# Kernel tuning notes

Hardware: AMD Instinct MI355X
Metric: run time of the kernel (lower is better)

Reference implementation:

```python
import jax, jax.numpy as jnp
import numpy as np

N = 16384      # total atoms (8 proteins x ~2048)
E = 524288     # N * max_neighbors(32)
B = 8          # graphs
F_IN = 26      # 20 residue types + 6 atom types
D = 128        # node_dim
H = 256        # hidden_dim
OUT = 64       # output_dim
L = 4          # n_layers
N_RBF = 16
CUTOFF = 10.0


def setup_inputs() -> dict:
    key = jax.random.key(0)
    ks = jax.random.split(key, 24)
    s = 0.05
    inp = {
        "positions": jax.random.normal(ks[0], (N, 3), jnp.float32) * 10.0,
        "node_features": jax.random.normal(ks[1], (N, F_IN), jnp.float32),
        "edge_index": jax.random.randint(ks[2], (2, E), 0, N, jnp.int32),
        "batch": jnp.sort(jax.random.randint(ks[3], (N,), 0, B, jnp.int32)),
        # node embedding MLP
        "emb_W1": jax.random.normal(ks[4], (F_IN, D), jnp.float32) * s,
        "emb_b1": jnp.zeros((D,), jnp.float32),
        "emb_W2": jax.random.normal(ks[5], (D, D), jnp.float32) * s,
        "emb_b2": jnp.zeros((D,), jnp.float32),
        # per-layer message MLP: [2D + n_rbf] -> H -> D
        "msg_W1": jax.random.normal(ks[6], (L, 2 * D + N_RBF, H), jnp.float32) * s,
        "msg_b1": jnp.zeros((L, H), jnp.float32),
        "msg_W2": jax.random.normal(ks[7], (L, H, D), jnp.float32) * s,
        "msg_b2": jnp.zeros((L, D), jnp.float32),
        # per-layer update MLP: [2D] -> H -> D (residual)
        "upd_W1": jax.random.normal(ks[8], (L, 2 * D, H), jnp.float32) * s,
        "upd_b1": jnp.zeros((L, H), jnp.float32),
        "upd_W2": jax.random.normal(ks[9], (L, H, D), jnp.float32) * s,
        "upd_b2": jnp.zeros((L, D), jnp.float32),
        # readout MLP: D -> H -> OUT
        "r_W1": jax.random.normal(ks[10], (D, H), jnp.float32) * s,
        "r_b1": jnp.zeros((H,), jnp.float32),
        "r_W2": jax.random.normal(ks[11], (H, OUT), jnp.float32) * s,
        "r_b2": jnp.zeros((OUT,), jnp.float32),
    }
    return inp


def _mlp2(x, W1, b1, W2, b2):
    return jax.nn.silu(x @ W1 + b1) @ W2 + b2


def _edge_rbf(positions, src, dst):
    rel = positions[dst] - positions[src]                      # (E,3)
    d = jnp.sqrt(jnp.sum(rel * rel, axis=-1) + 1e-12)          # (E,)
    centers = jnp.linspace(0.0, CUTOFF, N_RBF, dtype=positions.dtype)
    width = CUTOFF / N_RBF
    rbf = jnp.exp(-((d[:, None] - centers) ** 2) / (2.0 * width * width))  # (E,n_rbf)
    env = 0.5 * (jnp.cos(jnp.pi * d / CUTOFF) + 1.0) * (d < CUTOFF)        # cosine cutoff
    return rbf * env[:, None]


def reference(positions, node_features, edge_index, batch,
              emb_W1, emb_b1, emb_W2, emb_b2,
              msg_W1, msg_b1, msg_W2, msg_b2,
              upd_W1, upd_b1, upd_W2, upd_b2,
              r_W1, r_b1, r_W2, r_b2):
    src, dst = edge_index[0], edge_index[1]
    h = _mlp2(node_features, emb_W1, emb_b1, emb_W2, emb_b2)   # (N,D)
    ef = _edge_rbf(positions, src, dst)                        # (E,n_rbf)
    for i in range(L):
        m_in = jnp.concatenate([h[src], h[dst], ef], axis=-1)  # (E,2D+n_rbf)
        m = _mlp2(m_in, msg_W1[i], msg_b1[i], msg_W2[i], msg_b2[i])  # (E,D)
        agg = jax.ops.segment_sum(m, dst, num_segments=N)      # (N,D)
        u_in = jnp.concatenate([h, agg], axis=-1)              # (N,2D)
        h = h + _mlp2(u_in, upd_W1[i], upd_b1[i], upd_W2[i], upd_b2[i])
    # mean readout per graph
    counts = jax.ops.segment_sum(jnp.ones((N,), h.dtype), batch, num_segments=B)
    g = jax.ops.segment_sum(h, batch, num_segments=B) / jnp.maximum(counts, 1.0)[:, None]
    return _mlp2(g, r_W1, r_b1, r_W2, r_b2)                    # (B,OUT)
```

## Files before the change

### kernel.cpp

```cpp
#include <hip/hip_runtime.h>
#include <math.h>

#define NATOMS 16384
#define NEDGES 524288
#define NLAYERS 4
#define TE 64

typedef __bf16 bf16x8 __attribute__((ext_vector_type(8)));
typedef __bf16 bf16x4 __attribute__((ext_vector_type(4)));
typedef float f32x4 __attribute__((ext_vector_type(4)));

__device__ __forceinline__ float silu_f(float x) {
  return x * __builtin_amdgcn_rcpf(1.0f + __expf(-x));
}

__global__ __launch_bounds__(256) void hist_kernel(
    const int* __restrict__ dst, int* __restrict__ counts)
{
  int e = blockIdx.x * 256 + threadIdx.x;
  atomicAdd(&counts[dst[e]], 1);
}

__global__ __launch_bounds__(1024) void scan_kernel(
    const int* __restrict__ counts, int* __restrict__ cursor)
{
  __shared__ int buf[1024];
  __shared__ int carry_s;
  int tid = threadIdx.x;
  if (tid == 0) carry_s = 0;
  __syncthreads();
  for (int c = 0; c < 16; c++) {
    int v = counts[c * 1024 + tid];
    buf[tid] = v;
    __syncthreads();
    for (int off = 1; off < 1024; off <<= 1) {
      int t = (tid >= off) ? buf[tid - off] : 0;
      __syncthreads();
      buf[tid] += t;
      __syncthreads();
    }
    cursor[c * 1024 + tid] = buf[tid] - v + carry_s;
    __syncthreads();
    if (tid == 1023) carry_s += buf[1023];
    __syncthreads();
  }
}

__global__ __launch_bounds__(256) void scatter_kernel(
    const int* __restrict__ src, const int* __restrict__ dst,
    int* __restrict__ cursor, int* __restrict__ esrc, int* __restrict__ edst)
{
  int e = blockIdx.x * 256 + threadIdx.x;
  int d = dst[e];
  int p = atomicAdd(&cursor[d], 1);
  esrc[p] = src[e];
  edst[p] = d;
}

__global__ __launch_bounds__(256) void degf_kernel(
    const int* __restrict__ counts, float* __restrict__ degf)
{
  int n = blockIdx.x * 256 + threadIdx.x;
  degf[n] = (float)counts[n];
}

__global__ __launch_bounds__(256) void conv_t_kernel(
    const float* __restrict__ W, __bf16* __restrict__ Wt,
    int ldN, int k0, int Kin, int Kpad, long lsrc, long ldst)
{
  long l = blockIdx.y;
  int i = blockIdx.x * 256 + threadIdx.x;
  int n = i / Kpad, k = i - n * Kpad;
  float v = (k < Kin) ? W[l * lsrc + (size_t)(k0 + k) * ldN + n] : 0.0f;
  Wt[l * ldst + (size_t)n * Kpad + k] = (__bf16)v;
}

__global__ __launch_bounds__(256) void build_b2c_kernel(
    const float* __restrict__ mW1, __bf16* __restrict__ Bc)
{
  long l = blockIdx.y;
  int i = blockIdx.x * 256 + threadIdx.x;
  int c = i >> 5, k = i & 31;
  float v = (k < 16) ? mW1[l * (272L * 256) + (size_t)(256 + k) * 256 + c] : 0.0f;
  Bc[l * (256L * 32) + i] = (__bf16)v;
}

__global__ __launch_bounds__(256) void w2u_kernel(
    const float* __restrict__ mW2, const float* __restrict__ uW1,
    float* __restrict__ W2u)
{
  long l = blockIdx.y;
  int r = blockIdx.x, c = threadIdx.x;
  float acc = 0.0f;
  for (int k = 0; k < 128; k++)
    acc += mW2[(l * 256 + r) * 128 + k] *
           uW1[l * 65536 + (size_t)(128 + k) * 256 + c];
  W2u[(l * 256 + r) * 256 + c] = acc;
}

__global__ __launch_bounds__(256) void b2u_kernel(
    const float* __restrict__ mb2, const float* __restrict__ uW1,
    float* __restrict__ b2u)
{
  long l = blockIdx.x;
  int c = threadIdx.x;
  float acc = 0.0f;
  for (int k = 0; k < 128; k++)
    acc += mb2[l * 128 + k] * uW1[l * 65536 + (size_t)(128 + k) * 256 + c];
  b2u[l * 256 + c] = acc;
}

__global__ __launch_bounds__(256) void build_uw1ft_kernel(
    const float* __restrict__ uW1, const float* __restrict__ W2u,
    __bf16* __restrict__ Wt)
{
  long l = blockIdx.y;
  int i = blockIdx.x * 256 + threadIdx.x;
  int n = i / 384, k = i - n * 384;
  float v = (k < 128) ? uW1[l * 65536 + (size_t)k * 256 + n]
                      : W2u[l * 65536 + (size_t)(k - 128) * 256 + n];
  Wt[l * (256L * 384) + i] = (__bf16)v;
}

__global__ __launch_bounds__(128) void embed_kernel(
    const float* __restrict__ x, const float* __restrict__ W1,
    const float* __restrict__ b1, const float* __restrict__ W2,
    const float* __restrict__ b2, float* __restrict__ h,
    __bf16* __restrict__ hb)
{
  int n = blockIdx.x;
  int j = threadIdx.x;
  __shared__ float xs[26];
  __shared__ float hid[128];
  if (j < 26) xs[j] = x[n * 26 + j];
  __syncthreads();
  float acc = b1[j];
  #pragma unroll
  for (int k = 0; k < 26; k++) acc += xs[k] * W1[k * 128 + j];
  hid[j] = silu_f(acc);
  __syncthreads();
  float acc2 = b2[j];
  #pragma unroll 8
  for (int k = 0; k < 128; k++) acc2 += hid[k] * W2[k * 128 + j];
  h[(size_t)n * 128 + j] = acc2;
  hb[(size_t)n * 128 + j] = (__bf16)acc2;
}

__global__ __launch_bounds__(256) void rbf_kernel(
    const float* __restrict__ pos, const int* __restrict__ esrc,
    const int* __restrict__ edst, __bf16* __restrict__ efb)
{
  int e = blockIdx.x * 256 + threadIdx.x;
  int s = esrc[e], d = edst[e];
  float dx = pos[d * 3 + 0] - pos[s * 3 + 0];
  float dy = pos[d * 3 + 1] - pos[s * 3 + 1];
  float dz = pos[d * 3 + 2] - pos[s * 3 + 2];
  float dist = sqrtf(dx * dx + dy * dy + dz * dz + 1e-12f);
  float env = (dist < 10.0f)
                  ? 0.5f * (cosf(3.14159265358979f * dist * 0.1f) + 1.0f)
                  : 0.0f;
  bf16x8 o0, o1;
  #pragma unroll
  for (int i = 0; i < 16; i++) {
    float c = (10.0f / 15.0f) * (float)i;
    float t = dist - c;
    float v = env * __expf(-t * t * 1.28f);
    if (i < 8) o0[i] = (__bf16)v; else o1[i - 8] = (__bf16)v;
  }
  *(bf16x8*)(efb + (size_t)e * 16 + 0) = o0;
  *(bf16x8*)(efb + (size_t)e * 16 + 8) = o1;
}

__global__ __launch_bounds__(256) void zprep_kernel(
    const __bf16* __restrict__ hb, const float* __restrict__ b1,
    const __bf16* __restrict__ W1at, const __bf16* __restrict__ W1bt,
    __bf16* __restrict__ z1b, __bf16* __restrict__ z2b, float* __restrict__ aggH)
{
  __shared__ __bf16 s_n[64][136];
  int tid = threadIdx.x, n0 = blockIdx.x * 64;
  {
    int n = tid >> 2, t4 = tid & 3;
    const bf16x8* hr = (const bf16x8*)(hb + (size_t)(n0 + n) * 128);
    #pragma unroll
    for (int i = 0; i < 4; i++)
      *(bf16x8*)&s_n[n][t4 * 8 + 32 * i] = hr[t4 + 4 * i];
  }
  {
    float4 zz = make_float4(0.f, 0.f, 0.f, 0.f);
    float4* ap = (float4*)(aggH + (size_t)n0 * 256);
    for (int i = tid; i < 64 * 256 / 4; i += 256) ap[i] = zz;
  }
  __syncthreads();
  const int wv = tid >> 6, ln = tid & 63, lc = ln & 15, qd = ln >> 4;
  for (int cp = 0; cp < 2; cp++) {
    f32x4 aA[4][2], aB[4][2];
    #pragma unroll
    for (int nt = 0; nt < 2; nt++) {
      float bv = b1[cp * 128 + wv * 32 + nt * 16 + lc];
      #pragma unroll
      for (int mt = 0; mt < 4; mt++) {
        aA[mt][nt][0] = 0.f; aA[mt][nt][1] = 0.f;
        aA[mt][nt][2] = 0.f; aA[mt][nt][3] = 0.f;
        aB[mt][nt][0] = bv; aB[mt][nt][1] = bv;
        aB[mt][nt][2] = bv; aB[mt][nt][3] = bv;
      }
    }
    #pragma unroll
    for (int kt = 0; kt < 4; kt++) {
      bf16x8 af[4];
      #pragma unroll
      for (int mt = 0; mt < 4; mt++)
        af[mt] = *(const bf16x8*)&s_n[mt * 16 + lc][kt * 32 + qd * 8];
      bf16x8 bwA[2], bwB[2];
      #pragma unroll
      for (int nt = 0; nt < 2; nt++) {
        int c = cp * 128 + wv * 32 + nt * 16 + lc;
        bwA[nt] = *(const bf16x8*)(W1at + (size_t)c * 128 + kt * 32 + qd * 8);
        bwB[nt] = *(const bf16x8*)(W1bt + (size_t)c * 128 + kt * 32 + qd * 8);
      }
      #pragma unroll
      for (int mt = 0; mt < 4; mt++)
        #pragma unroll
        for (int nt = 0; nt < 2; nt++) {
          aA[mt][nt] = __builtin_amdgcn_mfma_f32_16x16x32_bf16(af[mt], bwA[nt], aA[mt][nt], 0, 0, 0);
          aB[mt][nt] = __builtin_amdgcn_mfma_f32_16x16x32_bf16(af[mt], bwB[nt], aB[mt][nt], 0, 0, 0);
        }
    }
    #pragma unroll
    for (int mt = 0; mt < 4; mt++)
      #pragma unroll
      for (int nt = 0; nt < 2; nt++) {
        int c = cp * 128 + wv * 32 + nt * 16 + lc;
        #pragma unroll
        for (int r = 0; r < 4; r++) {
          int n = n0 + mt * 16 + qd * 4 + r;
          z1b[(size_t)n * 256 + c] = (__bf16)aA[mt][nt][r];
          z2b[(size_t)n * 256 + c] = (__bf16)aB[mt][nt][r];
        }
      }
  }
}

#define MS_EF_OFF   33792
#define MS_SRC_OFF  36864
#define MS_DST_OFF  37120
#define MS_MASK_OFF 37376
#define MS_BYTES    37392

__global__ __launch_bounds__(256, 4) void msg_mfma_kernel(
    const __bf16* __restrict__ z1b, const __bf16* __restrict__ z2b,
    const __bf16* __restrict__ efb,
    const int* __restrict__ esrc, const int* __restrict__ edst,
    const __bf16* __restrict__ B2c, float* __restrict__ aggH)
{
  __shared__ __align__(16) char smem[MS_BYTES];
  float (*s_hT)[66] = (float(*)[66])(smem);
  __bf16 (*s_ef)[24] = (__bf16(*)[24])(smem + MS_EF_OFF);
  int* s_src = (int*)(smem + MS_SRC_OFF);
  int* s_dst = (int*)(smem + MS_DST_OFF);
  unsigned int* s_mask = (unsigned int*)(smem + MS_MASK_OFF);

  int tid = threadIdx.x, e0 = blockIdx.x * TE;

  if (tid < TE) {
    int d = edst[e0 + tid];
    s_dst[tid] = d;
    int dp = (tid == 0) ? (d ^ 1) : edst[e0 + tid - 1];
    unsigned long long mb = __ballot(d != dp);
    if (tid == 0) { s_mask[0] = (unsigned int)mb; s_mask[1] = (unsigned int)(mb >> 32); }
  } else if (tid < 2 * TE) {
    s_src[tid - TE] = esrc[e0 + tid - TE];
  }
  {
    int e = tid >> 2, t4 = tid & 3;
    if (t4 < 2)
      *(bf16x8*)&s_ef[e][t4 * 8] =
          *(const bf16x8*)(efb + (size_t)(e0 + e) * 16 + t4 * 8);
  }
  __syncthreads();

  const int wv = tid >> 6, ln = tid & 63, lc = ln & 15, qd = ln >> 4;
  const unsigned int mlo = __builtin_amdgcn_readfirstlane(s_mask[0]);
  const unsigned int mhi = __builtin_amdgcn_readfirstlane(s_mask[1]);

  bf16x8 bI;
  #pragma unroll
  for (int j = 0; j < 8; j++)
    bI[j] = (__bf16)((lc == (qd & 1) * 8 + j) ? 1.0f : 0.0f);

  const __bf16* pz[4];
  #pragma unroll
  for (int mt = 0; mt < 4; mt++) {
    int m = mt * 16 + lc;
    int row = (qd < 2) ? s_src[m] : s_dst[m];
    pz[mt] = ((qd < 2) ? z1b : z2b) + (size_t)row * 256 + (qd & 1) * 8;
  }
  const int jcol = tid & 127, r0 = (tid >> 7) * 32;

  for (int hf = 0; hf < 2; hf++) {
    const int cb = hf * 128 + wv * 32;
    bf16x8 bw[2];
    #pragma unroll
    for (int nt = 0; nt < 2; nt++)
      bw[nt] = *(const bf16x8*)(B2c + (size_t)(cb + nt * 16 + lc) * 32 + qd * 8);

    #pragma unroll
    for (int mt = 0; mt < 4; mt++) {
      bf16x8 aef = *(const bf16x8*)&s_ef[mt * 16 + lc][(qd & 1) * 8];
      #pragma unroll
      for (int nt = 0; nt < 2; nt++) {
        bf16x8 az = *(const bf16x8*)(pz[mt] + cb + nt * 16);
        f32x4 z; z[0] = 0.f; z[1] = 0.f; z[2] = 0.f; z[3] = 0.f;
        f32x4 acc = __builtin_amdgcn_mfma_f32_16x16x32_bf16(az, bI, z, 0, 0, 0);
        acc = __builtin_amdgcn_mfma_f32_16x16x32_bf16(aef, bw[nt], acc, 0, 0, 0);
        float2 p0, p1;
        p0.x = silu_f(acc[0]); p0.y = silu_f(acc[1]);
        p1.x = silu_f(acc[2]); p1.y = silu_f(acc[3]);
        float* wp = &s_hT[wv * 32 + nt * 16 + lc][mt * 16 + qd * 4];
        *(float2*)wp = p0;
        *(float2*)(wp + 2) = p1;
      }
    }
    __syncthreads();

    {
      float2 v[16];
      #pragma unroll
      for (int c = 0; c < 16; c++)
        v[c] = *(const float2*)&s_hT[jcol][r0 + c * 2];
      float acc = 0.0f;
      int cur = s_dst[r0];
      #pragma unroll
      for (int i = 0; i < 32; i++) {
        int m = r0 + i;
        bool bnd = (m < 32) ? ((mlo >> m) & 1u) : ((mhi >> (m - 32)) & 1u);
        if (i > 0 && bnd) {
          atomicAdd(&aggH[(size_t)cur * 256 + hf * 128 + jcol], acc);
          acc = 0.0f;
          cur = s_dst[m];
        }
        acc += (i & 1) ? v[i >> 1].y : v[i >> 1].x;
      }
      atomicAdd(&aggH[(size_t)cur * 256 + hf * 128 + jcol], acc);
    }
    __syncthreads();
  }
}

__global__ __launch_bounds__(256, 2) void upd_mfma_kernel(
    float* __restrict__ h, __bf16* __restrict__ hb,
    float* __restrict__ aggH, const float* __restrict__ degf,
    const __bf16* __restrict__ uW1ft, const float* __restrict__ b1,
    const float* __restrict__ b2u,
    const __bf16* __restrict__ uW2t, const float* __restrict__ b2,
    int do_z, const float* __restrict__ nb1,
    const __bf16* __restrict__ nW1at, const __bf16* __restrict__ nW1bt,
    __bf16* __restrict__ z1b, __bf16* __restrict__ z2b)
{
  __shared__ __bf16 s_u[64][392];
  __shared__ __bf16 s_uh[64][136];
  int tid = threadIdx.x, n0 = blockIdx.x * 64;
  {
    int n = tid >> 2, t4 = tid & 3;
    const bf16x8* hr = (const bf16x8*)(hb + (size_t)(n0 + n) * 128);
    #pragma unroll
    for (int i = 0; i < 4; i++)
      *(bf16x8*)&s_u[n][t4 * 8 + 32 * i] = hr[t4 + 4 * i];
    const float* sr = aggH + (size_t)(n0 + n) * 256;
    #pragma unroll
    for (int i = 0; i < 8; i++) {
      int col = t4 * 8 + i * 32;
      float4 a = *(const float4*)(sr + col);
      float4 b = *(const float4*)(sr + col + 4);
      bf16x8 o;
      o[0] = (__bf16)a.x; o[1] = (__bf16)a.y; o[2] = (__bf16)a.z; o[3] = (__bf16)a.w;
      o[4] = (__bf16)b.x; o[5] = (__bf16)b.y; o[6] = (__bf16)b.z; o[7] = (__bf16)b.w;
      *(bf16x8*)&s_u[n][128 + col] = o;
    }
  }
  __syncthreads();
  const int wv = tid >> 6, ln = tid & 63, lc = ln & 15, qd = ln >> 4;

  float dg[4][4];
  #pragma unroll
  for (int mt = 0; mt < 4; mt++)
    #pragma unroll
    for (int r = 0; r < 4; r++)
      dg[mt][r] = degf[n0 + mt * 16 + qd * 4 + r];

  f32x4 acc2[4][2];
  #pragma unroll
  for (int nt = 0; nt < 2; nt++) {
    float bv = b2[wv * 32 + nt * 16 + lc];
    #pragma unroll
    for (int mt = 0; mt < 4; mt++) {
      acc2[mt][nt][0] = bv; acc2[mt][nt][1] = bv;
      acc2[mt][nt][2] = bv; acc2[mt][nt][3] = bv;
    }
  }

  for (int hf = 0; hf < 2; hf++) {
    f32x4 acc1[4][2];
    #pragma unroll
    for (int nt = 0; nt < 2; nt++) {
      int c = hf * 128 + wv * 32 + nt * 16 + lc;
      float bv = b1[c];
      float b2uv = b2u[c];
      #pragma unroll
      for (int mt = 0; mt < 4; mt++)
        #pragma unroll
        for (int r = 0; r < 4; r++)
          acc1[mt][nt][r] = bv + dg[mt][r] * b2uv;
    }
    #pragma unroll
    for (int kt = 0; kt < 12; kt++) {
      bf16x8 af[4];
      #pragma unroll
      for (int mt = 0; mt < 4; mt++)
        af[mt] = *(const bf16x8*)&s_u[mt * 16 + lc][kt * 32 + qd * 8];
      bf16x8 bw[2];
      #pragma unroll
      for (int nt = 0; nt < 2; nt++)
        bw[nt] = *(const bf16x8*)(uW1ft +
                 (size_t)(hf * 128 + wv * 32 + nt * 16 + lc) * 384 + kt * 32 + qd * 8);
      #pragma unroll
      for (int mt = 0; mt < 4; mt++)
        #pragma unroll
        for (int nt = 0; nt < 2; nt++)
          acc1[mt][nt] = __builtin_amdgcn_mfma_f32_16x16x32_bf16(af[mt], bw[nt], acc1[mt][nt], 0, 0, 0);
    }
    __syncthreads();
    #pragma unroll
    for (int mt = 0; mt < 4; mt++)
      #pragma unroll
      for (int nt = 0; nt < 2; nt++) {
        int cc = wv * 32 + nt * 16 + lc;
        #pragma unroll
        for (int r = 0; r < 4; r++)
          s_uh[mt * 16 + qd * 4 + r][cc] = (__bf16)silu_f(acc1[mt][nt][r]);
      }
    __syncthreads();
    #pragma unroll
    for (int kt = 0; kt < 4; kt++) {
      bf16x8 a2[4];
      #pragma unroll
      for (int mt = 0; mt < 4; mt++)
        a2[mt] = *(const bf16x8*)&s_uh[mt * 16 + lc][kt * 32 + qd * 8];
      bf16x8 b2w[2];
      #pragma unroll
      for (int nt = 0; nt < 2; nt++)
        b2w[nt] = *(const bf16x8*)(uW2t +
                  (size_t)(wv * 32 + nt * 16 + lc) * 256 + hf * 128 + kt * 32 + qd * 8);
      #pragma unroll
      for (int mt = 0; mt < 4; mt++)
        #pragma unroll
        for (int nt = 0; nt < 2; nt++)
          acc2[mt][nt] = __builtin_amdgcn_mfma_f32_16x16x32_bf16(a2[mt], b2w[nt], acc2[mt][nt], 0, 0, 0);
    }
  }

  #pragma unroll
  for (int mt = 0; mt < 4; mt++)
    #pragma unroll
    for (int nt = 0; nt < 2; nt++) {
      int c = wv * 32 + nt * 16 + lc;
      #pragma unroll
      for (int r = 0; r < 4; r++) {
        int n = n0 + mt * 16 + qd * 4 + r;
        float v = h[(size_t)n * 128 + c] + acc2[mt][nt][r];
        h[(size_t)n * 128 + c] = v;
        hb[(size_t)n * 128 + c] = (__bf16)v;
      }
    }

  if (do_z) {
    __syncthreads();
    {
      float4 zz = make_float4(0.f, 0.f, 0.f, 0.f);
      float4* ap = (float4*)(aggH + (size_t)n0 * 256);
      for (int i = tid; i < 64 * 256 / 4; i += 256) ap[i] = zz;
      int n = tid >> 2, t4 = tid & 3;
      const bf16x8* hr = (const bf16x8*)(hb + (size_t)(n0 + n) * 128);
      #pragma unroll
      for (int i = 0; i < 4; i++)
        *(bf16x8*)&s_u[n][t4 * 8 + 32 * i] = hr[t4 + 4 * i];
    }
    __syncthreads();
    for (int cp = 0; cp < 2; cp++) {
      f32x4 aA[4][2], aB[4][2];
      #pragma unroll
      for (int nt = 0; nt < 2; nt++) {
        float bv = nb1[cp * 128 + wv * 32 + nt * 16 + lc];
        #pragma unroll
        for (int mt = 0; mt < 4; mt++) {
          aA[mt][nt][0] = 0.f; aA[mt][nt][1] = 0.f;
          aA[mt][nt][2] = 0.f; aA[mt][nt][3] = 0.f;
          aB[mt][nt][0] = bv; aB[mt][nt][1] = bv;
          aB[mt][nt][2] = bv; aB[mt][nt][3] = bv;
        }
      }
      #pragma unroll
      for (int kt = 0; kt < 4; kt++) {
        bf16x8 af[4];
        #pragma unroll
        for (int mt = 0; mt < 4; mt++)
          af[mt] = *(const bf16x8*)&s_u[mt * 16 + lc][kt * 32 + qd * 8];
        bf16x8 bwA[2], bwB[2];
        #pragma unroll
        for (int nt = 0; nt < 2; nt++) {
          int c = cp * 128 + wv * 32 + nt * 16 + lc;
          bwA[nt] = *(const bf16x8*)(nW1at + (size_t)c * 128 + kt * 32 + qd * 8);
          bwB[nt] = *(const bf16x8*)(nW1bt + (size_t)c * 128 + kt * 32 + qd * 8);
        }
        #pragma unroll
        for (int mt = 0; mt < 4; mt++)
          #pragma unroll
          for (int nt = 0; nt < 2; nt++) {
            aA[mt][nt] = __builtin_amdgcn_mfma_f32_16x16x32_bf16(af[mt], bwA[nt], aA[mt][nt], 0, 0, 0);
            aB[mt][nt] = __builtin_amdgcn_mfma_f32_16x16x32_bf16(af[mt], bwB[nt], aB[mt][nt], 0, 0, 0);
          }
      }
      #pragma unroll
      for (int mt = 0; mt < 4; mt++)
        #pragma unroll
        for (int nt = 0; nt < 2; nt++) {
          int c = cp * 128 + wv * 32 + nt * 16 + lc;
          #pragma unroll
          for (int r = 0; r < 4; r++) {
            int n = n0 + mt * 16 + qd * 4 + r;
            z1b[(size_t)n * 256 + c] = (__bf16)aA[mt][nt][r];
            z2b[(size_t)n * 256 + c] = (__bf16)aB[mt][nt][r];
          }
        }
    }
  }
}

__global__ __launch_bounds__(128) void readout_sum_kernel(
    const float* __restrict__ h, const int* __restrict__ batch,
    float* __restrict__ gsum, float* __restrict__ gcnt)
{
  int j = threadIdx.x;
  int n0 = blockIdx.x * 128;
  float acc = 0.f, cacc = 0.f;
  int cur = batch[n0];
  for (int i = 0; i < 128; i++) {
    int b = batch[n0 + i];
    if (b != cur) {
      atomicAdd(&gsum[cur * 128 + j], acc);
      if (j == 0) atomicAdd(&gcnt[cur], cacc);
      acc = 0.f; cacc = 0.f; cur = b;
    }
    acc += h[(size_t)(n0 + i) * 128 + j];
    cacc += 1.f;
  }
  atomicAdd(&gsum[cur * 128 + j], acc);
  if (j == 0) atomicAdd(&gcnt[cur], cacc);
}

__global__ __launch_bounds__(256) void readout_mlp_kernel(
    const float* __restrict__ gsum, const float* __restrict__ gcnt,
    const float* __restrict__ W1, const float* __restrict__ b1,
    const float* __restrict__ W2, const float* __restrict__ b2,
    float* __restrict__ out)
{
  __shared__ float g[8][128];
  __shared__ float hid[8][256];
  int tid = threadIdx.x;
  for (int i = tid; i < 8 * 128; i += 256) {
    int b = i >> 7, c = i & 127;
    g[b][c] = gsum[i] / fmaxf(gcnt[b], 1.0f);
  }
  __syncthreads();
  {
    float bb = b1[tid];
    float a[8];
    #pragma unroll
    for (int b = 0; b < 8; b++) a[b] = bb;
    for (int k = 0; k < 128; k++) {
      float w = W1[k * 256 + tid];
      #pragma unroll
      for (int b = 0; b < 8; b++) a[b] += g[b][k] * w;
    }
    #pragma unroll
    for (int b = 0; b < 8; b++) hid[b][tid] = silu_f(a[b]);
  }
  __syncthreads();
  int j = tid & 63, bg = tid >> 6;
  float a0 = b2[j], a1 = b2[j];
  for (int k = 0; k < 256; k++) {
    float w = W2[k * 64 + j];
    a0 += hid[bg * 2 + 0][k] * w;
    a1 += hid[bg * 2 + 1][k] * w;
  }
  out[(bg * 2 + 0) * 64 + j] = a0;
  out[(bg * 2 + 1) * 64 + j] = a1;
}

extern "C" void kernel_launch(void* const* d_in, const int* in_sizes, int n_in,
                              void* d_out, int out_size, void* d_ws, size_t ws_size,
                              hipStream_t stream) {
  const float* pos   = (const float*)d_in[0];
  const float* xfeat = (const float*)d_in[1];
  const int*   eidx  = (const int*)d_in[2];
  const int*   batch = (const int*)d_in[3];
  const float* eW1 = (const float*)d_in[4];
  const float* eb1 = (const float*)d_in[5];
  const float* eW2 = (const float*)d_in[6];
  const float* eb2 = (const float*)d_in[7];
  const float* mW1 = (const float*)d_in[8];
  const float* mb1 = (const float*)d_in[9];
  const float* mW2 = (const float*)d_in[10];
  const float* mb2 = (const float*)d_in[11];
  const float* uW1 = (const float*)d_in[12];
  const float* ub1 = (const float*)d_in[13];
  const float* uW2 = (const float*)d_in[14];
  const float* ub2 = (const float*)d_in[15];
  const float* rW1 = (const float*)d_in[16];
  const float* rb1 = (const float*)d_in[17];
  const float* rW2 = (const float*)d_in[18];
  const float* rb2 = (const float*)d_in[19];

  const int* srcI = eidx;
  const int* dstI = eidx + NEDGES;

  char* base = (char*)d_ws;
  float* h    = (float*)base;  base += (size_t)NATOMS * 128 * 4;
  float* aggH = (float*)base;  base += (size_t)NATOMS * 256 * 4;
  __bf16* z1b = (__bf16*)base; base += (size_t)NATOMS * 256 * 2;
  __bf16* z2b = (__bf16*)base; base += (size_t)NATOMS * 256 * 2;
  __bf16* hb  = (__bf16*)base; base += (size_t)NATOMS * 128 * 2;
  __bf16* efb = (__bf16*)base; base += (size_t)NEDGES * 16 * 2;
  __bf16* W1at = (__bf16*)base; base += (size_t)NLAYERS * 256 * 128 * 2;
  __bf16* W1bt = (__bf16*)base; base += (size_t)NLAYERS * 256 * 128 * 2;
  __bf16* B2c  = (__bf16*)base; base += (size_t)NLAYERS * 256 * 32 * 2;
  __bf16* uW1ft = (__bf16*)base; base += (size_t)NLAYERS * 256 * 384 * 2;
  __bf16* uW2t = (__bf16*)base; base += (size_t)NLAYERS * 128 * 256 * 2;
  float* W2u  = (float*)base;  base += (size_t)NLAYERS * 256 * 256 * 4;
  float* b2u  = (float*)base;  base += (size_t)NLAYERS * 256 * 4;
  float* degf = (float*)base;  base += (size_t)NATOMS * 4;
  float* gsum = (float*)base;  base += 8 * 128 * 4;
  float* gcnt = (float*)base;  base += 8 * 4;
  int* counts = (int*)base;    base += (size_t)NATOMS * 4;
  int* cursor = (int*)base;    base += (size_t)NATOMS * 4;
  int* esrc   = (int*)base;    base += (size_t)NEDGES * 4;
  int* edst   = (int*)base;    base += (size_t)NEDGES * 4;

  hipMemsetAsync(counts, 0, NATOMS * sizeof(int), stream);
  hist_kernel<<<NEDGES / 256, 256, 0, stream>>>(dstI, counts);
  scan_kernel<<<1, 1024, 0, stream>>>(counts, cursor);
  scatter_kernel<<<NEDGES / 256, 256, 0, stream>>>(srcI, dstI, cursor, esrc, edst);
  degf_kernel<<<NATOMS / 256, 256, 0, stream>>>(counts, degf);

  conv_t_kernel<<<dim3(128, NLAYERS), 256, 0, stream>>>(mW1, W1at, 256,   0, 128, 128, 272L*256, 256L*128);
  conv_t_kernel<<<dim3(128, NLAYERS), 256, 0, stream>>>(mW1, W1bt, 256, 128, 128, 128, 272L*256, 256L*128);
  build_b2c_kernel<<<dim3(32, NLAYERS), 256, 0, stream>>>(mW1, B2c);
  w2u_kernel<<<dim3(256, NLAYERS), 256, 0, stream>>>(mW2, uW1, W2u);
  b2u_kernel<<<NLAYERS, 256, 0, stream>>>(mb2, uW1, b2u);
  build_uw1ft_kernel<<<dim3(384, NLAYERS), 256, 0, stream>>>(uW1, W2u, uW1ft);
  conv_t_kernel<<<dim3(128, NLAYERS), 256, 0, stream>>>(uW2, uW2t, 128,   0, 256, 256, 256L*128, 128L*256);

  embed_kernel<<<NATOMS, 128, 0, stream>>>(xfeat, eW1, eb1, eW2, eb2, h, hb);
  rbf_kernel<<<NEDGES / 256, 256, 0, stream>>>(pos, esrc, edst, efb);

  zprep_kernel<<<NATOMS / 64, 256, 0, stream>>>(
      hb, mb1, W1at, W1bt, z1b, z2b, aggH);

  for (int l = 0; l < NLAYERS; l++) {
    int ln = (l < NLAYERS - 1) ? (l + 1) : l;
    msg_mfma_kernel<<<NEDGES / TE, 256, 0, stream>>>(
        z1b, z2b, efb, esrc, edst,
        B2c + (size_t)l * 256 * 32, aggH);
    upd_mfma_kernel<<<NATOMS / 64, 256, 0, stream>>>(
        h, hb, aggH, degf,
        uW1ft + (size_t)l * 256 * 384, ub1 + (size_t)l * 256,
        b2u + (size_t)l * 256,
        uW2t + (size_t)l * 128 * 256, ub2 + (size_t)l * 128,
        (l < NLAYERS - 1) ? 1 : 0,
        mb1 + (size_t)ln * 256,
        W1at + (size_t)ln * 256 * 128, W1bt + (size_t)ln * 256 * 128,
        z1b, z2b);
  }

  hipMemsetAsync(gsum, 0, (8 * 128 + 8) * sizeof(float), stream);
  readout_sum_kernel<<<NATOMS / 128, 128, 0, stream>>>(h, batch, gsum, gcnt);
  readout_mlp_kernel<<<1, 256, 0, stream>>>(gsum, gcnt, rW1, rb1, rW2, rb2,
                                            (float*)d_out);
}
```

Measured before the change: 715.0 us.

## Merge weight-prep kernels, fold degree into scan, prefetch z rows, shrink upd LDS

Seven weight preparation kernels are merged into one block-partitioned prep kernel, and the W2u intermediate buffer is dropped by computing it inline. The scan now does a single-pass blocked prefix sum that also writes degf, which removes a kernel. The message kernel preloads all z gather loads into registers before the MFMA loop. The update kernel reads h directly from global memory instead of staging it in LDS, which cuts LDS use so occupancy can rise to 3 blocks. The aims are fewer launches and better latency hiding, at the cost of more registers and uncached global reads in the update GEMM.

```diff
diff --git a/kernel.cpp b/kernel.cpp
--- a/kernel.cpp
+++ b/kernel.cpp
@@ -22,27 +22,37 @@
 }
 
 __global__ __launch_bounds__(1024) void scan_kernel(
-    const int* __restrict__ counts, int* __restrict__ cursor)
-{
-  __shared__ int buf[1024];
-  __shared__ int carry_s;
+    const int* __restrict__ counts, int* __restrict__ cursor,
+    float* __restrict__ degf)
+{
+  __shared__ int s_tot[1024];
   int tid = threadIdx.x;
-  if (tid == 0) carry_s = 0;
-  __syncthreads();
-  for (int c = 0; c < 16; c++) {
-    int v = counts[c * 1024 + tid];
-    buf[tid] = v;
+  int v[16];
+  {
+    const int4* cp = (const int4*)(counts + tid * 16);
+    int4 a = cp[0], b = cp[1], c = cp[2], d = cp[3];
+    v[0]=a.x; v[1]=a.y; v[2]=a.z; v[3]=a.w;
+    v[4]=b.x; v[5]=b.y; v[6]=b.z; v[7]=b.w;
+    v[8]=c.x; v[9]=c.y; v[10]=c.z; v[11]=c.w;
+    v[12]=d.x; v[13]=d.y; v[14]=d.z; v[15]=d.w;
+  }
+  int tot = 0;
+  #pragma unroll
+  for (int i = 0; i < 16; i++) tot += v[i];
+  s_tot[tid] = tot;
+  __syncthreads();
+  for (int off = 1; off < 1024; off <<= 1) {
+    int t = (tid >= off) ? s_tot[tid - off] : 0;
     __syncthreads();
-    for (int off = 1; off < 1024; off <<= 1) {
-      int t = (tid >= off) ? buf[tid - off] : 0;
-      __syncthreads();
-      buf[tid] += t;
-      __syncthreads();
-    }
-    cursor[c * 1024 + tid] = buf[tid] - v + carry_s;
+    s_tot[tid] += t;
     __syncthreads();
-    if (tid == 1023) carry_s += buf[1023];
-    __syncthreads();
+  }
+  int run = s_tot[tid] - tot;
+  #pragma unroll
+  for (int i = 0; i < 16; i++) {
+    cursor[tid * 16 + i] = run;
+    degf[tid * 16 + i] = (float)v[i];
+    run += v[i];
   }
 }
 
@@ -57,69 +67,53 @@
   edst[p] = d;
 }
 
-__global__ __launch_bounds__(256) void degf_kernel(
-    const int* __restrict__ counts, float* __restrict__ degf)
-{
-  int n = blockIdx.x * 256 + threadIdx.x;
-  degf[n] = (float)counts[n];
-}
-
-__global__ __launch_bounds__(256) void conv_t_kernel(
-    const float* __restrict__ W, __bf16* __restrict__ Wt,
-    int ldN, int k0, int Kin, int Kpad, long lsrc, long ldst)
+__global__ __launch_bounds__(256) void prep_kernel(
+    const float* __restrict__ mW1, const float* __restrict__ mW2,
+    const float* __restrict__ uW1, const float* __restrict__ uW2,
+    const float* __restrict__ mb2,
+    __bf16* __restrict__ W1at, __bf16* __restrict__ W1bt,
+    __bf16* __restrict__ B2c, __bf16* __restrict__ uW1ft,
+    __bf16* __restrict__ uW2t, float* __restrict__ b2u)
 {
   long l = blockIdx.y;
-  int i = blockIdx.x * 256 + threadIdx.x;
-  int n = i / Kpad, k = i - n * Kpad;
-  float v = (k < Kin) ? W[l * lsrc + (size_t)(k0 + k) * ldN + n] : 0.0f;
-  Wt[l * ldst + (size_t)n * Kpad + k] = (__bf16)v;
-}
-
-__global__ __launch_bounds__(256) void build_b2c_kernel(
-    const float* __restrict__ mW1, __bf16* __restrict__ Bc)
-{
-  long l = blockIdx.y;
-  int i = blockIdx.x * 256 + threadIdx.x;
-  int c = i >> 5, k = i & 31;
-  float v = (k < 16) ? mW1[l * (272L * 256) + (size_t)(256 + k) * 256 + c] : 0.0f;
-  Bc[l * (256L * 32) + i] = (__bf16)v;
-}
-
-__global__ __launch_bounds__(256) void w2u_kernel(
-    const float* __restrict__ mW2, const float* __restrict__ uW1,
-    float* __restrict__ W2u)
-{
-  long l = blockIdx.y;
-  int r = blockIdx.x, c = threadIdx.x;
-  float acc = 0.0f;
-  for (int k = 0; k < 128; k++)
-    acc += mW2[(l * 256 + r) * 128 + k] *
-           uW1[l * 65536 + (size_t)(128 + k) * 256 + c];
-  W2u[(l * 256 + r) * 256 + c] = acc;
-}
-
-__global__ __launch_bounds__(256) void b2u_kernel(
-    const float* __restrict__ mb2, const float* __restrict__ uW1,
-    float* __restrict__ b2u)
-{
-  long l = blockIdx.x;
-  int c = threadIdx.x;
-  float acc = 0.0f;
-  for (int k = 0; k < 128; k++)
-    acc += mb2[l * 128 + k] * uW1[l * 65536 + (size_t)(128 + k) * 256 + c];
-  b2u[l * 256 + c] = acc;
-}
-
-__global__ __launch_bounds__(256) void build_uw1ft_kernel(
-    const float* __restrict__ uW1, const float* __restrict__ W2u,
-    __bf16* __restrict__ Wt)
-{
-  long l = blockIdx.y;
-  int i = blockIdx.x * 256 + threadIdx.x;
-  int n = i / 384, k = i - n * 384;
-  float v = (k < 128) ? uW1[l * 65536 + (size_t)k * 256 + n]
-                      : W2u[l * 65536 + (size_t)(k - 128) * 256 + n];
-  Wt[l * (256L * 384) + i] = (__bf16)v;
+  int bx = blockIdx.x, tid = threadIdx.x;
+  if (bx < 128) {
+    int i = bx * 256 + tid;
+    int n = i >> 7, k = i & 127;
+    W1at[l * (256L * 128) + i] = (__bf16)mW1[l * (272L * 256) + (size_t)k * 256 + n];
+  } else if (bx < 256) {
+    int i = (bx - 128) * 256 + tid;
+    int n = i >> 7, k = i & 127;
+    W1bt[l * (256L * 128) + i] = (__bf16)mW1[l * (272L * 256) + (size_t)(128 + k) * 256 + n];
+  } else if (bx < 288) {
+    int i = (bx - 256) * 256 + tid;
+    int c = i >> 5, k = i & 31;
+    float v = (k < 16) ? mW1[l * (272L * 256) + (size_t)(256 + k) * 256 + c] : 0.0f;
+    B2c[l * (256L * 32) + i] = (__bf16)v;
+  } else if (bx < 672) {
+    int i = (bx - 288) * 256 + tid;
+    int n = i / 384, k = i - n * 384;
+    float v;
+    if (k < 128) {
+      v = uW1[l * 65536 + (size_t)k * 256 + n];
+    } else {
+      int r = k - 128;
+      v = 0.0f;
+      for (int j = 0; j < 128; j++)
+        v += mW2[(l * 256 + r) * 128 + j] * uW1[l * 65536 + (size_t)(128 + j) * 256 + n];
+    }
+    uW1ft[l * (256L * 384) + i] = (__bf16)v;
+  } else if (bx < 800) {
+    int i = (bx - 672) * 256 + tid;
+    int n = i >> 8, k = i & 255;
+    uW2t[l * (128L * 256) + i] = (__bf16)uW2[l * (256L * 128) + (size_t)k * 128 + n];
+  } else {
+    int c = tid;
+    float acc = 0.0f;
+    for (int j = 0; j < 128; j++)
+      acc += mb2[l * 128 + j] * uW1[l * 65536 + (size_t)(128 + j) * 256 + c];
+    b2u[l * 256 + c] = acc;
+  }
 }
 
 __global__ __launch_bounds__(128) void embed_kernel(
@@ -288,15 +282,27 @@
   for (int j = 0; j < 8; j++)
     bI[j] = (__bf16)((lc == (qd & 1) * 8 + j) ? 1.0f : 0.0f);
 
-  const __bf16* pz[4];
-  #pragma unroll
-  for (int mt = 0; mt < 4; mt++) {
-    int m = mt * 16 + lc;
-    int row = (qd < 2) ? s_src[m] : s_dst[m];
-    pz[mt] = ((qd < 2) ? z1b : z2b) + (size_t)row * 256 + (qd & 1) * 8;
-  }
+  bf16x8 za[2][4][2];
+  {
+    const __bf16* pz[4];
+    #pragma unroll
+    for (int mt = 0; mt < 4; mt++) {
+      int m = mt * 16 + lc;
+      int row = (qd < 2) ? s_src[m] : s_dst[m];
+      pz[mt] = ((qd < 2) ? z1b : z2b) + (size_t)row * 256 + (qd & 1) * 8;
+    }
+    #pragma unroll
+    for (int hf = 0; hf < 2; hf++)
+      #pragma unroll
+      for (int mt = 0; mt < 4; mt++)
+        #pragma unroll
+        for (int nt = 0; nt < 2; nt++)
+          za[hf][mt][nt] = *(const bf16x8*)(pz[mt] + hf * 128 + wv * 32 + nt * 16);
+  }
+
   const int jcol = tid & 127, r0 = (tid >> 7) * 32;
 
+  #pragma unroll
   for (int hf = 0; hf < 2; hf++) {
     const int cb = hf * 128 + wv * 32;
     bf16x8 bw[2];
@@ -309,9 +315,8 @@
       bf16x8 aef = *(const bf16x8*)&s_ef[mt * 16 + lc][(qd & 1) * 8];
       #pragma unroll
       for (int nt = 0; nt < 2; nt++) {
-        bf16x8 az = *(const bf16x8*)(pz[mt] + cb + nt * 16);
         f32x4 z; z[0] = 0.f; z[1] = 0.f; z[2] = 0.f; z[3] = 0.f;
-        f32x4 acc = __builtin_amdgcn_mfma_f32_16x16x32_bf16(az, bI, z, 0, 0, 0);
+        f32x4 acc = __builtin_amdgcn_mfma_f32_16x16x32_bf16(za[hf][mt][nt], bI, z, 0, 0, 0);
         acc = __builtin_amdgcn_mfma_f32_16x16x32_bf16(aef, bw[nt], acc, 0, 0, 0);
         float2 p0, p1;
         p0.x = silu_f(acc[0]); p0.y = silu_f(acc[1]);
@@ -347,7 +352,7 @@
   }
 }
 
-__global__ __launch_bounds__(256, 2) void upd_mfma_kernel(
+__global__ __launch_bounds__(256, 3) void upd_mfma_kernel(
     float* __restrict__ h, __bf16* __restrict__ hb,
     float* __restrict__ aggH, const float* __restrict__ degf,
     const __bf16* __restrict__ uW1ft, const float* __restrict__ b1,
@@ -357,15 +362,11 @@
     const __bf16* __restrict__ nW1at, const __bf16* __restrict__ nW1bt,
     __bf16* __restrict__ z1b, __bf16* __restrict__ z2b)
 {
-  __shared__ __bf16 s_u[64][392];
+  __shared__ __bf16 s_s[64][264];
   __shared__ __bf16 s_uh[64][136];
   int tid = threadIdx.x, n0 = blockIdx.x * 64;
   {
     int n = tid >> 2, t4 = tid & 3;
-    const bf16x8* hr = (const bf16x8*)(hb + (size_t)(n0 + n) * 128);
-    #pragma unroll
-    for (int i = 0; i < 4; i++)
-      *(bf16x8*)&s_u[n][t4 * 8 + 32 * i] = hr[t4 + 4 * i];
     const float* sr = aggH + (size_t)(n0 + n) * 256;
     #pragma unroll
     for (int i = 0; i < 8; i++) {
@@ -375,11 +376,16 @@
       bf16x8 o;
       o[0] = (__bf16)a.x; o[1] = (__bf16)a.y; o[2] = (__bf16)a.z; o[3] = (__bf16)a.w;
       o[4] = (__bf16)b.x; o[5] = (__bf16)b.y; o[6] = (__bf16)b.z; o[7] = (__bf16)b.w;
-      *(bf16x8*)&s_u[n][128 + col] = o;
+      *(bf16x8*)&s_s[n][col] = o;
     }
   }
   __syncthreads();
   const int wv = tid >> 6, ln = tid & 63, lc = ln & 15, qd = ln >> 4;
+
+  const __bf16* ph[4];
+  #pragma unroll
+  for (int mt = 0; mt < 4; mt++)
+    ph[mt] = hb + (size_t)(n0 + mt * 16 + lc) * 128 + qd * 8;
 
   float dg[4][4];
   #pragma unroll
@@ -417,7 +423,9 @@
       bf16x8 af[4];
       #pragma unroll
       for (int mt = 0; mt < 4; mt++)
-        af[mt] = *(const bf16x8*)&s_u[mt * 16 + lc][kt * 32 + qd * 8];
+        af[mt] = (kt < 4)
+            ? *(const bf16x8*)(ph[mt] + kt * 32)
+            : *(const bf16x8*)&s_s[mt * 16 + lc][(kt - 4) * 32 + qd * 8];
       bf16x8 bw[2];
       #pragma unroll
       for (int nt = 0; nt < 2; nt++)
@@ -479,13 +487,7 @@
       float4 zz = make_float4(0.f, 0.f, 0.f, 0.f);
       float4* ap = (float4*)(aggH + (size_t)n0 * 256);
       for (int i = tid; i < 64 * 256 / 4; i += 256) ap[i] = zz;
-      int n = tid >> 2, t4 = tid & 3;
-      const bf16x8* hr = (const bf16x8*)(hb + (size_t)(n0 + n) * 128);
-      #pragma unroll
-      for (int i = 0; i < 4; i++)
-        *(bf16x8*)&s_u[n][t4 * 8 + 32 * i] = hr[t4 + 4 * i];
-    }
-    __syncthreads();
+    }
     for (int cp = 0; cp < 2; cp++) {
       f32x4 aA[4][2], aB[4][2];
       #pragma unroll
@@ -504,7 +506,7 @@
         bf16x8 af[4];
         #pragma unroll
         for (int mt = 0; mt < 4; mt++)
-          af[mt] = *(const bf16x8*)&s_u[mt * 16 + lc][kt * 32 + qd * 8];
+          af[mt] = *(const bf16x8*)(ph[mt] + kt * 32);
         bf16x8 bwA[2], bwB[2];
         #pragma unroll
         for (int nt = 0; nt < 2; nt++) {
@@ -636,7 +638,6 @@
   __bf16* B2c  = (__bf16*)base; base += (size_t)NLAYERS * 256 * 32 * 2;
   __bf16* uW1ft = (__bf16*)base; base += (size_t)NLAYERS * 256 * 384 * 2;
   __bf16* uW2t = (__bf16*)base; base += (size_t)NLAYERS * 128 * 256 * 2;
-  float* W2u  = (float*)base;  base += (size_t)NLAYERS * 256 * 256 * 4;
   float* b2u  = (float*)base;  base += (size_t)NLAYERS * 256 * 4;
   float* degf = (float*)base;  base += (size_t)NATOMS * 4;
   float* gsum = (float*)base;  base += 8 * 128 * 4;
@@ -648,17 +649,11 @@
 
   hipMemsetAsync(counts, 0, NATOMS * sizeof(int), stream);
   hist_kernel<<<NEDGES / 256, 256, 0, stream>>>(dstI, counts);
-  scan_kernel<<<1, 1024, 0, stream>>>(counts, cursor);
+  scan_kernel<<<1, 1024, 0, stream>>>(counts, cursor, degf);
   scatter_kernel<<<NEDGES / 256, 256, 0, stream>>>(srcI, dstI, cursor, esrc, edst);
-  degf_kernel<<<NATOMS / 256, 256, 0, stream>>>(counts, degf);
-
-  conv_t_kernel<<<dim3(128, NLAYERS), 256, 0, stream>>>(mW1, W1at, 256,   0, 128, 128, 272L*256, 256L*128);
-  conv_t_kernel<<<dim3(128, NLAYERS), 256, 0, stream>>>(mW1, W1bt, 256, 128, 128, 128, 272L*256, 256L*128);
-  build_b2c_kernel<<<dim3(32, NLAYERS), 256, 0, stream>>>(mW1, B2c);
-  w2u_kernel<<<dim3(256, NLAYERS), 256, 0, stream>>>(mW2, uW1, W2u);
-  b2u_kernel<<<NLAYERS, 256, 0, stream>>>(mb2, uW1, b2u);
-  build_uw1ft_kernel<<<dim3(384, NLAYERS), 256, 0, stream>>>(uW1, W2u, uW1ft);
-  conv_t_kernel<<<dim3(128, NLAYERS), 256, 0, stream>>>(uW2, uW2t, 128,   0, 256, 256, 256L*128, 128L*256);
+
+  prep_kernel<<<dim3(801, NLAYERS), 256, 0, stream>>>(
+      mW1, mW2, uW1, uW2, mb2, W1at, W1bt, B2c, uW1ft, uW2t, b2u);
 
   embed_kernel<<<NATOMS, 128, 0, stream>>>(xfeat, eW1, eb1, eW2, eb2, h, hb);
   rbf_kernel<<<NEDGES / 256, 256, 0, stream>>>(pos, esrc, edst, efb);
```

After: 720.2 us. About the same (+0.7%).
